# Kernel tuning notes

Measured on AMD Instinct MI355X. Metric: run time of the kernel, lower is better.

## Reference

```python
import jax, jax.numpy as jnp
import numpy as np
import math

B, S, H = 2, 2048, 3072
N_HEADS, N_KV_HEADS, HEAD_DIM = 32, 8, 96
ROPE_THETA = 10000.0
OP_SIZE = N_HEADS * HEAD_DIM + 2 * N_KV_HEADS * HEAD_DIM  # 4608


def setup_inputs() -> dict:
    key = jax.random.key(0)
    k1, k2, k3 = jax.random.split(key, 3)
    hidden_states = jax.random.normal(k1, (B, S, H), dtype=jnp.float32)
    # additive causal mask: 0 on/below diagonal, -inf-ish above
    neg = jnp.finfo(jnp.float32).min
    causal = jnp.where(jnp.tril(jnp.ones((S, S), dtype=bool)), 0.0, neg)
    attention_mask = jnp.broadcast_to(causal[None, None], (B, 1, S, S)).astype(jnp.float32)
    # torch nn.Linear convention: weight [out_features, in_features]
    w_qkv = jax.random.normal(k2, (OP_SIZE, H), dtype=jnp.float32) * 0.02
    w_o = jax.random.normal(k3, (H, H), dtype=jnp.float32) * 0.02
    position_ids = jnp.broadcast_to(jnp.arange(S, dtype=jnp.int32)[None], (B, S))
    return {"hidden_states": hidden_states, "attention_mask": attention_mask,
            "w_qkv": w_qkv, "w_o": w_o, "position_ids": position_ids}


def _rotate_half(x):
    half = x.shape[-1] // 2
    return jnp.concatenate([-x[..., half:], x[..., :half]], axis=-1)


def _rope_cos_sin(position_ids, head_dim, theta):
    # Phi3RotaryEmbedding (no scaling)
    inv_freq = 1.0 / (theta ** (jnp.arange(0, head_dim, 2, dtype=jnp.float32) / head_dim))
    freqs = position_ids.astype(jnp.float32)[:, :, None] * inv_freq[None, None, :]  # [b,s,d/2]
    emb = jnp.concatenate([freqs, freqs], axis=-1)  # [b,s,d]
    return jnp.cos(emb), jnp.sin(emb)


def reference(hidden_states, attention_mask, w_qkv, w_o, position_ids):
    b, s, _ = hidden_states.shape
    qkv = jnp.einsum('bsh,oh->bso', hidden_states, w_qkv)  # quantized qkv_proj (fp emulation)
    q_pos = N_HEADS * HEAD_DIM
    kv_pos = q_pos + N_KV_HEADS * HEAD_DIM
    q = qkv[..., :q_pos].reshape(b, s, N_HEADS, HEAD_DIM).transpose(0, 2, 1, 3)
    k = qkv[..., q_pos:kv_pos].reshape(b, s, N_KV_HEADS, HEAD_DIM).transpose(0, 2, 1, 3)
    v = qkv[..., kv_pos:].reshape(b, s, N_KV_HEADS, HEAD_DIM).transpose(0, 2, 1, 3)

    cos, sin = _rope_cos_sin(position_ids, HEAD_DIM, ROPE_THETA)
    cos, sin = cos[:, None], sin[:, None]  # [b,1,s,d]
    q = q * cos + _rotate_half(q) * sin
    k = k * cos + _rotate_half(k) * sin

    # repeat_kv: GQA expand kv heads to query heads
    groups = N_HEADS // N_KV_HEADS
    k = jnp.repeat(k, groups, axis=1)  # [b,h,s,d]
    v = jnp.repeat(v, groups, axis=1)

    # quantized QK^T matmul (fp emulation)
    scores = jnp.einsum('bhqd,bhkd->bhqk', q, k) / math.sqrt(HEAD_DIM)
    scores = scores + attention_mask  # additive causal mask
    attn = jax.nn.softmax(scores.astype(jnp.float32), axis=-1).astype(v.dtype)
    # dropout p=0 (eval); quantized attn @ V matmul (fp emulation)
    out = jnp.einsum('bhqk,bhkd->bhqd', attn, v)
    out = out.transpose(0, 2, 1, 3).reshape(b, s, N_HEADS * HEAD_DIM)
    out = jnp.einsum('bso,ho->bsh', out, w_o)  # quantized o_proj
    return out
```

## Files before the change

kernel.cpp:

```cpp
#include <hip/hip_runtime.h>
#include <hip/hip_bf16.h>
#include <math.h>

#define S_LEN 2048
#define HDIM  3072
#define NH    32
#define NKV   8
#define HD    96
#define OPSZ  4608
#define QPOS  3072
#define KPOS  3840

typedef short  short8 __attribute__((ext_vector_type(8)));
typedef short  short4v __attribute__((ext_vector_type(4)));
typedef float  f32x4  __attribute__((ext_vector_type(4)));
typedef unsigned short us4 __attribute__((ext_vector_type(4)));

typedef __attribute__((address_space(1))) const unsigned int* gas1_t;
typedef __attribute__((address_space(3))) unsigned int* las3_t;

__device__ __forceinline__ void gl_lds16(const void* g, void* l) {
  __builtin_amdgcn_global_load_lds((gas1_t)g, (las3_t)l, 16, 0, 0);
}

#define VMCNT(n) asm volatile("s_waitcnt vmcnt(" #n ")" ::: "memory")

__device__ __forceinline__ unsigned short f2b(float f) {
  union { float f; unsigned u; } x; x.f = f;
  unsigned r = x.u + 0x7fffu + ((x.u >> 16) & 1u);
  return (unsigned short)(r >> 16);
}
__device__ __forceinline__ float b2f(unsigned short b) {
  union { unsigned u; float f; } x; x.u = ((unsigned)b) << 16;
  return x.f;
}

__device__ __forceinline__ short4v pack_bf16_4(float p0, float p1, float p2, float p3) {
  unsigned u0 = __builtin_bit_cast(unsigned, p0) + 0x8000u;
  unsigned u1 = __builtin_bit_cast(unsigned, p1) + 0x8000u;
  unsigned u2 = __builtin_bit_cast(unsigned, p2) + 0x8000u;
  unsigned u3 = __builtin_bit_cast(unsigned, p3) + 0x8000u;
  unsigned lo = __builtin_amdgcn_perm(u1, u0, 0x07060302u);
  unsigned hi = __builtin_amdgcn_perm(u3, u2, 0x07060302u);
  uint2 q; q.x = lo; q.y = hi;
  return __builtin_bit_cast(short4v, q);
}

__global__ __launch_bounds__(256) void k_convert3(const float* __restrict__ s0, int n0,
                                                  const float* __restrict__ s1, int n1,
                                                  const float* __restrict__ s2, int n2,
                                                  unsigned short* __restrict__ dst) {
  int i = blockIdx.x * 256 + threadIdx.x;
  const float* src; int local;
  if (i < n0)            { src = s0; local = i; }
  else if (i < n0 + n1)  { src = s1; local = i - n0; }
  else if (i < n0 + n1 + n2) { src = s2; local = i - n0 - n1; }
  else return;
  float4 v = ((const float4*)src)[local];
  us4 o;
  o[0] = f2b(v.x); o[1] = f2b(v.y); o[2] = f2b(v.z); o[3] = f2b(v.w);
  ((us4*)dst)[i] = o;
}

template<int OUTBF, int NF>
__global__ __launch_bounds__(512, 2) void k_gemm_pipe(const unsigned short* __restrict__ A,
                                                      const unsigned short* __restrict__ Bt,
                                                      void* __restrict__ Cout,
                                                      int M, int N, int K, int GX) {
  constexpr int BN    = NF * 32;
  constexpr int GSLOT = 8192 + BN * 32;
  __shared__ unsigned short lds[4 * GSLOT];

  const int NC = K >> 5;
  const int tid = threadIdx.x;
  const int lane = tid & 63;
  const int wave = tid >> 6;
  const int wm = wave & 3, wn = wave >> 2;
  const int lr = lane & 15, lg = lane >> 4;
  const int prh = lr >> 1, bit = lr & 1;

  const int nwg = gridDim.x;
  const int id  = blockIdx.x;
  const int sw  = (id & 7) * (nwg >> 3) + (id >> 3);
  const int bx  = sw % GX, by = sw / GX;
  const int m0 = by * 256, n0 = bx * BN;

  const int i0 = tid, i1 = 512 + tid;
  const int p0 = i0 >> 3, g0 = (i0 & 7) ^ (p0 & 7);
  const int p1 = i1 >> 3, g1 = (i1 & 7) ^ (p1 & 7);
  const unsigned short* aG0 = A + (size_t)(m0 + 2 * p0 + (g0 >> 2)) * K + (g0 & 3) * 8;
  const unsigned short* aG1 = A + (size_t)(m0 + 2 * p1 + (g1 >> 2)) * K + (g1 & 3) * 8;
  const int aO0 = i0 * 8, aO1 = i1 * 8;

  const int q0 = i0 >> 3, h0 = (i0 & 7) ^ (q0 & 7);
  const int q1 = i1 >> 3, h1 = (i1 & 7) ^ (q1 & 7);
  const unsigned short* bG0 = Bt + (size_t)(n0 + 2 * q0 + (h0 >> 2)) * K + (h0 & 3) * 8;
  const unsigned short* bG1 = Bt + (size_t)(n0 + 2 * q1 + (h1 >> 2)) * K + (h1 & 3) * 8;
  const int bO0 = 8192 + i0 * 8, bO1 = 8192 + i1 * 8;
  const int i2 = 1024 + (tid & 127);
  const int q2 = i2 >> 3, h2 = (i2 & 7) ^ (q2 & 7);
  const unsigned short* bG2 = Bt + (size_t)(n0 + 2 * q2 + (h2 >> 2)) * K + (h2 & 3) * 8;
  const int bO2 = 8192 + i2 * 8;
  const bool xb = (NF == 9) ? (tid < 128) : (tid < 256);

  auto stageA = [&](int c) {
    unsigned short* sb = &lds[(c & 3) * GSLOT];
    gl_lds16(aG0 + c * 32, sb + aO0);
    gl_lds16(aG1 + c * 32, sb + aO1);
  };
  auto stageB = [&](int c) {
    unsigned short* sb = &lds[(c & 3) * GSLOT];
    gl_lds16(bG0 + c * 32, sb + bO0);
    if constexpr (NF == 9) {
      gl_lds16(bG1 + c * 32, sb + bO1);
      if (xb) gl_lds16(bG2 + c * 32, sb + bO2);
    } else {
      if (xb) gl_lds16(bG1 + c * 32, sb + bO1);
    }
  };

  const int gp  = ((bit << 2) + lg) ^ prh;
  const int aRd = wm * 2048 + prh * 64 + gp * 8;
  const int bRd = 8192 + wn * (BN * 16) + prh * 64 + gp * 8;

  f32x4 acc[4][NF];
#pragma unroll
  for (int mf = 0; mf < 4; mf++)
#pragma unroll
    for (int nf = 0; nf < NF; nf++)
#pragma unroll
      for (int r = 0; r < 4; r++) acc[mf][nf][r] = 0.0f;

#define VM_STEADY() do { \
    if constexpr (NF == 9) { if (wave < 2) { VMCNT(10); } else { VMCNT(8); } } \
    else                   { if (wave < 4) { VMCNT(8);  } else { VMCNT(6); } } } while (0)
#define VM_TAIL1() do { \
    if constexpr (NF == 9) { if (wave < 2) { VMCNT(5); } else { VMCNT(4); } } \
    else                   { if (wave < 4) { VMCNT(4); } else { VMCNT(3); } } } while (0)

  stageA(0); stageB(0);
  stageA(1); stageB(1);
  stageA(2); stageB(2);
  VM_STEADY();
  __builtin_amdgcn_s_barrier();
  __builtin_amdgcn_sched_barrier(0);

  for (int c = 0; c < NC; ++c) {
    const unsigned short* sb = &lds[(c & 3) * GSLOT];
    short8 af[4], bf[NF];
#pragma unroll
    for (int mf = 0; mf < 4; mf++) af[mf] = *(const short8*)&sb[aRd + mf * 512];
#pragma unroll
    for (int nf = 0; nf < NF; nf++) bf[nf] = *(const short8*)&sb[bRd + nf * 512];
    if (c + 3 < NC) { stageA(c + 3); stageB(c + 3); }
    __builtin_amdgcn_s_setprio(1);
#pragma unroll
    for (int nf = 0; nf < NF; nf++)
#pragma unroll
      for (int mf = 0; mf < 4; mf++)
        acc[mf][nf] = __builtin_amdgcn_mfma_f32_16x16x32_bf16(af[mf], bf[nf], acc[mf][nf], 0, 0, 0);
    __builtin_amdgcn_s_setprio(0);
    if (c < NC - 3)       { VM_STEADY(); }
    else if (c == NC - 3) { VM_TAIL1(); }
    else if (c == NC - 2) { VMCNT(0); }
    if (c + 1 < NC) {
      __builtin_amdgcn_sched_barrier(0);
      __builtin_amdgcn_s_barrier();
      __builtin_amdgcn_sched_barrier(0);
    }
  }

#pragma unroll
  for (int mf = 0; mf < 4; mf++)
#pragma unroll
    for (int nf = 0; nf < NF; nf++)
#pragma unroll
      for (int r = 0; r < 4; r++) {
        int row = m0 + wm * 64 + mf * 16 + lg * 4 + r;
        int col = n0 + wn * (BN / 2) + nf * 16 + lr;
        if (OUTBF) ((unsigned short*)Cout)[(size_t)row * N + col] = f2b(acc[mf][nf][r]);
        else       ((float*)Cout)[(size_t)row * N + col] = acc[mf][nf][r];
      }
#undef VM_STEADY
#undef VM_TAIL1
}

__global__ __launch_bounds__(256) void k_rope(const unsigned short* __restrict__ qkv,
                                              const int* __restrict__ pos_ids,
                                              unsigned short* __restrict__ Qb,
                                              unsigned short* __restrict__ Kb) {
  __shared__ float cs[96], sn[96];
  int blk = blockIdx.x;
  int b = blk >> 11, s = blk & 2047;
  int t = threadIdx.x;
  int pos = pos_ids[blk];
  if (t < 48) {
    float e = -((float)(2 * t) / 96.0f) * 9.210340371976184f;
    float invf = __expf(e);
    float a = (float)pos * invf;
    float c, si;
    __sincosf(a, &si, &c);
    cs[t] = c; cs[t + 48] = c;
    sn[t] = si; sn[t + 48] = si;
  }
  __syncthreads();
  const unsigned short* row = qkv + (size_t)blk * OPSZ;
  const float qscale = 0.1020620726159658f;
  for (int o = t; o < KPOS; o += 256) {
    int d = o % 96;
    float x  = b2f(row[o]);
    float xp = b2f(row[d < 48 ? o + 48 : o - 48]);
    float rot = (d < 48) ? -xp : xp;
    float val = x * cs[d] + rot * sn[d];
    if (o < QPOS) {
      int h = o / 96;
      Qb[((size_t)(b * NH + h) * S_LEN + s) * HD + d] = f2b(val * qscale);
    } else {
      int kh = (o - QPOS) / 96;
      Kb[((size_t)(b * NKV + kh) * S_LEN + s) * HD + d] = f2b(val);
    }
  }
}

__global__ __launch_bounds__(256) void k_vtrans(const unsigned short* __restrict__ qkv,
                                                unsigned short* __restrict__ Vt) {
  int blk = blockIdx.x;
  int st = blk & 31, kh = (blk >> 5) & 7, b = blk >> 8;
  int s0 = st * 64;
  __shared__ unsigned short tile[96][65];
  int t = threadIdx.x;
#pragma unroll
  for (int c = 0; c < 24; c++) {
    int idx = c * 256 + t;
    int ls = idx / 96, d = idx % 96;
    tile[d][ls] = qkv[(size_t)(b * S_LEN + s0 + ls) * OPSZ + KPOS + kh * 96 + d];
  }
  __syncthreads();
#pragma unroll
  for (int c = 0; c < 24; c++) {
    int idx = c * 256 + t;
    int d = idx >> 6, ls = idx & 63;
    Vt[((size_t)(b * NKV + kh) * HD + d) * S_LEN + s0 + ls] = tile[d][ls];
  }
}

__global__ __launch_bounds__(512, 4) void k_flash(const unsigned short* __restrict__ Qb,
                                                  const unsigned short* __restrict__ Kb,
                                                  const unsigned short* __restrict__ Vt,
                                                  unsigned short* __restrict__ attn) {
  __shared__ unsigned short smem[36864];
  __shared__ float Lsh[128 * 8];
  unsigned short* QPs = smem + 24576;
  float* Osh = (float*)smem;

  int blk = blockIdx.x;
  int j = blk & 7;
  int h = (blk >> 3) & 31;
  int b = blk >> 8;
  int kh = h >> 2;
  int tid = threadIdx.x, lane = tid & 63, wave = tid >> 6;
  int lr = lane & 15, lg = lane >> 4;
  int qg = wave >> 1, kg = wave & 1;
  const int swz = (lr >> 1) & 3;

  const unsigned short* ksrc = Kb + (size_t)(b * NKV + kh) * S_LEN * HD;
  const unsigned short* vsrc = Vt + (size_t)(b * NKV + kh) * HD * S_LEN;

  auto stageKV = [&](int it, int sl) {
    int k0 = it * 64;
    unsigned short* Ksl = smem + sl * 6144;
    unsigned short* Vsl = smem + 12288 + sl * 6144;
#pragma unroll
    for (int p = 0; p < 3; p++) {
      int gi = p * 512 + tid;
      if (gi < 768) {
        int pl = gi >> 8, wp = gi & 255;
        int r = wp >> 2, s = wp & 3;
        int l = pl * 4 + (s ^ ((r >> 1) & 3));
        gl_lds16(ksrc + (size_t)(k0 + r) * HD + l * 8, &Ksl[gi * 8]);
      } else {
        int gi2 = gi - 768;
        int pl = (gi2 >= 384) ? 1 : 0;
        int rem = gi2 - pl * 384;
        int d = rem >> 2, s = rem & 3;
        int l = s ^ ((d >> 1) & 3);
        gl_lds16(vsrc + (size_t)d * S_LEN + k0 + pl * 32 + l * 8, &Vsl[gi2 * 8]);
      }
    }
  };

  for (int half = 0; half < 2; half++) {
    int qtile = half ? (15 - j) : j;
    int q0 = qtile * 128;
    const unsigned short* qsrc = Qb + ((size_t)(b * NH + h) * S_LEN + q0) * HD;
    int nk = qtile * 2 + 2;

    __syncthreads();
#pragma unroll
    for (int p = 0; p < 3; p++) {
      int gi = p * 512 + tid;
      int pl = gi >> 9, wp = gi & 511;
      int r = wp >> 2, s = wp & 3;
      int l = pl * 4 + (s ^ ((r >> 1) & 3));
      gl_lds16(qsrc + (size_t)r * HD + l * 8, &QPs[gi * 8]);
    }
    stageKV(0, 0);
    stageKV(1, 1);
    VMCNT(3);
    __builtin_amdgcn_s_barrier();
    __builtin_amdgcn_sched_barrier(0);

    short8 qf[2][3];
#pragma unroll
    for (int qt = 0; qt < 2; qt++)
#pragma unroll
      for (int ds = 0; ds < 3; ds++)
        qf[qt][ds] = *(const short8*)&QPs[ds * 4096 + (qg * 32 + qt * 16 + lr) * 32 + (lg ^ swz) * 8];

    f32x4 oacc[2][6];
#pragma unroll
    for (int qt = 0; qt < 2; qt++)
#pragma unroll
      for (int dt = 0; dt < 6; dt++)
#pragma unroll
        for (int r = 0; r < 4; r++) oacc[qt][dt][r] = 0.0f;
    float lsum[2] = {0.0f, 0.0f};

    for (int it = 0; it < nk; it++) {
      int sl = it & 1;
      const unsigned short* Ksl = smem + sl * 6144;
      const unsigned short* Vsl = smem + 12288 + sl * 6144;
      if (it >= 1 && it + 1 < nk) stageKV(it + 1, (it + 1) & 1);
      int k0 = it * 64;
      f32x4 sc[2][2];
#pragma unroll
      for (int kt = 0; kt < 2; kt++)
#pragma unroll
        for (int qt = 0; qt < 2; qt++)
#pragma unroll
          for (int r = 0; r < 4; r++) sc[kt][qt][r] = 0.0f;
#pragma unroll
      for (int kt = 0; kt < 2; kt++)
#pragma unroll
        for (int ds = 0; ds < 3; ds++) {
          short8 kf = *(const short8*)&Ksl[ds * 2048 + (kg * 32 + kt * 16 + lr) * 32 + (lg ^ swz) * 8];
#pragma unroll
          for (int qt = 0; qt < 2; qt++)
            sc[kt][qt] = __builtin_amdgcn_mfma_f32_16x16x32_bf16(kf, qf[qt][ds], sc[kt][qt], 0, 0, 0);
        }
      if (it >= nk - 2) {
#pragma unroll
        for (int kt = 0; kt < 2; kt++)
#pragma unroll
          for (int qt = 0; qt < 2; qt++) {
            int qrow = q0 + qg * 32 + qt * 16 + lr;
            int keyb = k0 + kg * 32 + kt * 16 + lg * 4;
#pragma unroll
            for (int r = 0; r < 4; r++)
              if (keyb + r > qrow) sc[kt][qt][r] = -3.0e38f;
          }
      }
      short4v pf[2][2];
#pragma unroll
      for (int kt = 0; kt < 2; kt++)
#pragma unroll
        for (int qt = 0; qt < 2; qt++) {
          float p0 = __expf(sc[kt][qt][0]);
          float p1 = __expf(sc[kt][qt][1]);
          float p2 = __expf(sc[kt][qt][2]);
          float p3 = __expf(sc[kt][qt][3]);
          lsum[qt] += (p0 + p1) + (p2 + p3);
          pf[kt][qt] = pack_bf16_4(p0, p1, p2, p3);
        }
#pragma unroll
      for (int kt = 0; kt < 2; kt++)
#pragma unroll
        for (int dt = 0; dt < 6; dt++) {
          short4v vf = *(const short4v*)&Vsl[kg * 3072 + (dt * 16 + lr) * 32 +
                                            (((kt * 2 + (lg >> 1)) ^ swz) * 8) + (lg & 1) * 4];
#pragma unroll
          for (int qt = 0; qt < 2; qt++)
            oacc[qt][dt] = __builtin_amdgcn_mfma_f32_16x16x16bf16_1k(pf[kt][qt], vf, oacc[qt][dt], 0, 0, 0);
        }
      VMCNT(0);
      __builtin_amdgcn_sched_barrier(0);
      __builtin_amdgcn_s_barrier();
      __builtin_amdgcn_sched_barrier(0);
    }
    if (kg == 0) {
#pragma unroll
      for (int qt = 0; qt < 2; qt++)
#pragma unroll
        for (int dt = 0; dt < 6; dt++)
#pragma unroll
          for (int r = 0; r < 4; r++)
            Osh[(qg * 32 + qt * 16 + lg * 4 + r) * 97 + dt * 16 + lr] = oacc[qt][dt][r];
    }
#pragma unroll
    for (int qt = 0; qt < 2; qt++)
      Lsh[(qg * 32 + qt * 16 + lr) * 8 + kg * 4 + lg] = lsum[qt];
    __syncthreads();
    if (kg == 1) {
      float linv[2][4];
#pragma unroll
      for (int qt = 0; qt < 2; qt++)
#pragma unroll
        for (int r = 0; r < 4; r++) {
          int row = qg * 32 + qt * 16 + lg * 4 + r;
          float4 a = *(const float4*)&Lsh[row * 8];
          float4 c = *(const float4*)&Lsh[row * 8 + 4];
          linv[qt][r] = 1.0f / ((a.x + a.y + a.z + a.w) + (c.x + c.y + c.z + c.w));
        }
#pragma unroll
      for (int qt = 0; qt < 2; qt++)
#pragma unroll
        for (int dt = 0; dt < 6; dt++)
#pragma unroll
          for (int r = 0; r < 4; r++) {
            int rowl = qg * 32 + qt * 16 + lg * 4 + r;
            float v = Osh[rowl * 97 + dt * 16 + lr] + oacc[qt][dt][r];
            int row = q0 + rowl;
            int col = h * 96 + dt * 16 + lr;
            attn[(size_t)(b * S_LEN + row) * HDIM + col] = f2b(v * linv[qt][r]);
          }
    }
  }
}

extern "C" void kernel_launch(void* const* d_in, const int* in_sizes, int n_in,
                              void* d_out, int out_size, void* d_ws, size_t ws_size,
                              hipStream_t stream) {
  const float* hidden = (const float*)d_in[0];
  const float* w_qkv  = (const float*)d_in[2];
  const float* w_o    = (const float*)d_in[3];
  const int*   posids = (const int*)d_in[4];

  const size_t M = 4096;
  unsigned short* hidden_bf = (unsigned short*)d_ws;
  unsigned short* wqkv_bf   = hidden_bf + M * HDIM;
  unsigned short* wo_bf     = wqkv_bf + (size_t)OPSZ * HDIM;
  unsigned short* qkv_bf    = wo_bf + (size_t)HDIM * HDIM;
  unsigned short* Qb   = hidden_bf;
  unsigned short* Kb   = wqkv_bf;
  unsigned short* Vt   = wqkv_bf + (size_t)NKV * 2 * S_LEN * HD;
  unsigned short* attn = qkv_bf;

  int n4h = (int)(M * HDIM / 4);
  int n4q = (int)((size_t)OPSZ * HDIM / 4);
  int n4o = (int)((size_t)HDIM * HDIM / 4);
  int n4t = n4h + n4q + n4o;
  k_convert3<<<(n4t + 255) / 256, 256, 0, stream>>>(hidden, n4h, w_qkv, n4q, w_o, n4o,
                                                    hidden_bf);

  k_gemm_pipe<1, 9><<<256, 512, 0, stream>>>(hidden_bf, wqkv_bf, qkv_bf,
                                             (int)M, OPSZ, HDIM, OPSZ / 288);
  k_rope<<<(int)M, 256, 0, stream>>>(qkv_bf, posids, Qb, Kb);
  k_vtrans<<<2 * NKV * (S_LEN / 64), 256, 0, stream>>>(qkv_bf, Vt);
  k_flash<<<2 * NH * 8, 512, 0, stream>>>(Qb, Kb, Vt, attn);
  k_gemm_pipe<0, 6><<<256, 512, 0, stream>>>(attn, wo_bf, d_out,
                                             (int)M, HDIM, HDIM, HDIM / 192);
}
```

Measured before the change: 482.3 us.

## Stagger GEMM MFMA clusters per wave and unroll flash loop by two

In the GEMM, waves in the two N halves now issue their MFMA work in opposite halves first, with matching B-fragment load order and sched barriers. The aim is to desynchronise the waves so LDS reads overlap MFMA execution. In the flash kernel, the KV loop is unrolled by two with fixed LDS buffer pointers, and the staging address arithmetic is precomputed into incrementing pointers and offset tables. This removes per-iteration index math and slot selection, at the cost of more registers and larger code.

New measurement: 509.2 us. 5.6% more time.

```diff
diff --git a/kernel.cpp b/kernel.cpp
--- a/kernel.cpp
+++ b/kernel.cpp
@@ -69,6 +69,7 @@
                                                       int M, int N, int K, int GX) {
   constexpr int BN    = NF * 32;
   constexpr int GSLOT = 8192 + BN * 32;
+  constexpr int NFA   = (NF + 1) / 2;
   __shared__ unsigned short lds[4 * GSLOT];
 
   const int NC = K >> 5;
@@ -138,6 +139,19 @@
     if constexpr (NF == 9) { if (wave < 2) { VMCNT(5); } else { VMCNT(4); } } \
     else                   { if (wave < 4) { VMCNT(4); } else { VMCNT(3); } } } while (0)
 
+#define CLUSTER_A() do { \
+    __builtin_amdgcn_s_setprio(1); \
+    _Pragma("unroll") for (int nf = 0; nf < NFA; nf++) \
+      _Pragma("unroll") for (int mf = 0; mf < 4; mf++) \
+        acc[mf][nf] = __builtin_amdgcn_mfma_f32_16x16x32_bf16(af[mf], bf[nf], acc[mf][nf], 0, 0, 0); \
+    __builtin_amdgcn_s_setprio(0); } while (0)
+#define CLUSTER_B() do { \
+    __builtin_amdgcn_s_setprio(1); \
+    _Pragma("unroll") for (int nf = NFA; nf < NF; nf++) \
+      _Pragma("unroll") for (int mf = 0; mf < 4; mf++) \
+        acc[mf][nf] = __builtin_amdgcn_mfma_f32_16x16x32_bf16(af[mf], bf[nf], acc[mf][nf], 0, 0, 0); \
+    __builtin_amdgcn_s_setprio(0); } while (0)
+
   stageA(0); stageB(0);
   stageA(1); stageB(1);
   stageA(2); stageB(2);
@@ -150,16 +164,26 @@
     short8 af[4], bf[NF];
 #pragma unroll
     for (int mf = 0; mf < 4; mf++) af[mf] = *(const short8*)&sb[aRd + mf * 512];
-#pragma unroll
-    for (int nf = 0; nf < NF; nf++) bf[nf] = *(const short8*)&sb[bRd + nf * 512];
+    if (wn == 0) {
+#pragma unroll
+      for (int nf = 0; nf < NF; nf++) bf[nf] = *(const short8*)&sb[bRd + nf * 512];
+    } else {
+#pragma unroll
+      for (int nf = NFA; nf < NF; nf++) bf[nf] = *(const short8*)&sb[bRd + nf * 512];
+#pragma unroll
+      for (int nf = 0; nf < NFA; nf++) bf[nf] = *(const short8*)&sb[bRd + nf * 512];
+    }
     if (c + 3 < NC) { stageA(c + 3); stageB(c + 3); }
-    __builtin_amdgcn_s_setprio(1);
-#pragma unroll
-    for (int nf = 0; nf < NF; nf++)
-#pragma unroll
-      for (int mf = 0; mf < 4; mf++)
-        acc[mf][nf] = __builtin_amdgcn_mfma_f32_16x16x32_bf16(af[mf], bf[nf], acc[mf][nf], 0, 0, 0);
-    __builtin_amdgcn_s_setprio(0);
+    __builtin_amdgcn_sched_barrier(0);
+    if (wn == 0) {
+      CLUSTER_A();
+      __builtin_amdgcn_sched_barrier(0);
+      CLUSTER_B();
+    } else {
+      CLUSTER_B();
+      __builtin_amdgcn_sched_barrier(0);
+      CLUSTER_A();
+    }
     if (c < NC - 3)       { VM_STEADY(); }
     else if (c == NC - 3) { VM_TAIL1(); }
     else if (c == NC - 2) { VMCNT(0); }
@@ -183,6 +207,8 @@
       }
 #undef VM_STEADY
 #undef VM_TAIL1
+#undef CLUSTER_A
+#undef CLUSTER_B
 }
 
 __global__ __launch_bounds__(256) void k_rope(const unsigned short* __restrict__ qkv,
@@ -250,7 +276,11 @@
                                                   unsigned short* __restrict__ attn) {
   __shared__ unsigned short smem[36864];
   __shared__ float Lsh[128 * 8];
-  unsigned short* QPs = smem + 24576;
+  unsigned short* const K0 = smem;
+  unsigned short* const K1 = smem + 6144;
+  unsigned short* const V0 = smem + 12288;
+  unsigned short* const V1 = smem + 18432;
+  unsigned short* const QPs = smem + 24576;
   float* Osh = (float*)smem;
 
   int blk = blockIdx.x;
@@ -266,34 +296,100 @@
   const unsigned short* ksrc = Kb + (size_t)(b * NKV + kh) * S_LEN * HD;
   const unsigned short* vsrc = Vt + (size_t)(b * NKV + kh) * HD * S_LEN;
 
-  auto stageKV = [&](int it, int sl) {
-    int k0 = it * 64;
-    unsigned short* Ksl = smem + sl * 6144;
-    unsigned short* Vsl = smem + 12288 + sl * 6144;
-#pragma unroll
-    for (int p = 0; p < 3; p++) {
-      int gi = p * 512 + tid;
-      if (gi < 768) {
-        int pl = gi >> 8, wp = gi & 255;
-        int r = wp >> 2, s = wp & 3;
-        int l = pl * 4 + (s ^ ((r >> 1) & 3));
-        gl_lds16(ksrc + (size_t)(k0 + r) * HD + l * 8, &Ksl[gi * 8]);
-      } else {
-        int gi2 = gi - 768;
-        int pl = (gi2 >= 384) ? 1 : 0;
-        int rem = gi2 - pl * 384;
-        int d = rem >> 2, s = rem & 3;
-        int l = s ^ ((d >> 1) & 3);
-        gl_lds16(vsrc + (size_t)d * S_LEN + k0 + pl * 32 + l * 8, &Vsl[gi2 * 8]);
-      }
-    }
-  };
+  const int gA = tid, plA = gA >> 8, wpA = gA & 255, rA = wpA >> 2, sA = wpA & 3;
+  const int lA = plA * 4 + (sA ^ ((rA >> 1) & 3));
+  const unsigned short* const kb0 = ksrc + (size_t)rA * HD + lA * 8;
+  const int rB = (tid & 255) >> 2, sB = tid & 3;
+  const int lB = 8 + (sB ^ ((rB >> 1) & 3));
+  const unsigned short* const kb1 = ksrc + (size_t)rB * HD + lB * 8;
+  const int gC = tid & 255, dC = gC >> 2, sC = gC & 3;
+  const int lC = sC ^ ((dC >> 1) & 3);
+  const unsigned short* const vb1 = vsrc + (size_t)dC * S_LEN + lC * 8;
+  const int gD = 256 + tid, plD = (gD >= 384) ? 1 : 0, remD = gD - plD * 384;
+  const int dD = remD >> 2, sD = remD & 3;
+  const int lD = sD ^ ((dD >> 1) & 3);
+  const unsigned short* const vb2 = vsrc + (size_t)dD * S_LEN + plD * 32 + lD * 8;
+  const int o0 = tid * 8, o1k = (512 + tid) * 8, o1v = (tid - 256) * 8, o2 = (256 + tid) * 8;
+
+  const unsigned short* kp0;
+  const unsigned short* kp1;
+  const unsigned short* vp1;
+  const unsigned short* vp2;
+
+#define FSTAGE(KD, VD) do {                                                   \
+    gl_lds16(kp0, (KD) + o0);                                                 \
+    if (tid < 256) gl_lds16(kp1, (KD) + o1k);                                 \
+    else           gl_lds16(vp1, (VD) + o1v);                                 \
+    gl_lds16(vp2, (VD) + o2);                                                 \
+    kp0 += 64 * HD; kp1 += 64 * HD; vp1 += 64; vp2 += 64;                     \
+  } while (0)
+
+  int koff[2][3], voff[2][6];
+#pragma unroll
+  for (int kt = 0; kt < 2; kt++) {
+#pragma unroll
+    for (int ds = 0; ds < 3; ds++)
+      koff[kt][ds] = ds * 2048 + (kg * 32 + kt * 16 + lr) * 32 + (lg ^ swz) * 8;
+#pragma unroll
+    for (int dt = 0; dt < 6; dt++)
+      voff[kt][dt] = kg * 3072 + (dt * 16 + lr) * 32 +
+                     (((kt * 2 + (lg >> 1)) ^ swz) * 8) + (lg & 1) * 4;
+  }
+
+#define FCOMP(KSL, VSL, IT, MASKED) do {                                      \
+    f32x4 sc[2][2];                                                           \
+    _Pragma("unroll") for (int kt = 0; kt < 2; kt++)                          \
+      _Pragma("unroll") for (int qt = 0; qt < 2; qt++)                        \
+        _Pragma("unroll") for (int r = 0; r < 4; r++) sc[kt][qt][r] = 0.0f;   \
+    _Pragma("unroll") for (int kt = 0; kt < 2; kt++)                          \
+      _Pragma("unroll") for (int ds = 0; ds < 3; ds++) {                      \
+        short8 kf = *(const short8*)&(KSL)[koff[kt][ds]];                     \
+        _Pragma("unroll") for (int qt = 0; qt < 2; qt++)                      \
+          sc[kt][qt] = __builtin_amdgcn_mfma_f32_16x16x32_bf16(kf, qf[qt][ds], sc[kt][qt], 0, 0, 0); \
+      }                                                                       \
+    if (MASKED) {                                                             \
+      int k0m = (IT) * 64;                                                    \
+      _Pragma("unroll") for (int kt = 0; kt < 2; kt++)                        \
+        _Pragma("unroll") for (int qt = 0; qt < 2; qt++) {                    \
+          int qrow = q0 + qg * 32 + qt * 16 + lr;                             \
+          int keyb = k0m + kg * 32 + kt * 16 + lg * 4;                        \
+          _Pragma("unroll") for (int r = 0; r < 4; r++)                       \
+            if (keyb + r > qrow) sc[kt][qt][r] = -3.0e38f;                    \
+        }                                                                     \
+    }                                                                         \
+    short4v pf[2][2];                                                         \
+    _Pragma("unroll") for (int kt = 0; kt < 2; kt++)                          \
+      _Pragma("unroll") for (int qt = 0; qt < 2; qt++) {                      \
+        float pp0 = __expf(sc[kt][qt][0]);                                    \
+        float pp1 = __expf(sc[kt][qt][1]);                                    \
+        float pp2 = __expf(sc[kt][qt][2]);                                    \
+        float pp3 = __expf(sc[kt][qt][3]);                                    \
+        lsum[qt] += (pp0 + pp1) + (pp2 + pp3);                                \
+        pf[kt][qt] = pack_bf16_4(pp0, pp1, pp2, pp3);                         \
+      }                                                                       \
+    _Pragma("unroll") for (int kt = 0; kt < 2; kt++)                          \
+      _Pragma("unroll") for (int dt = 0; dt < 6; dt++) {                      \
+        short4v vf = *(const short4v*)&(VSL)[voff[kt][dt]];                   \
+        _Pragma("unroll") for (int qt = 0; qt < 2; qt++)                      \
+          oacc[qt][dt] = __builtin_amdgcn_mfma_f32_16x16x16bf16_1k(pf[kt][qt], vf, oacc[qt][dt], 0, 0, 0); \
+      }                                                                       \
+  } while (0)
+
+#define FSYNC() do {                                                          \
+    VMCNT(0);                                                                 \
+    __builtin_amdgcn_sched_barrier(0);                                        \
+    __builtin_amdgcn_s_barrier();                                             \
+    __builtin_amdgcn_sched_barrier(0);                                        \
+  } while (0)
 
   for (int half = 0; half < 2; half++) {
     int qtile = half ? (15 - j) : j;
     int q0 = qtile * 128;
     const unsigned short* qsrc = Qb + ((size_t)(b * NH + h) * S_LEN + q0) * HD;
     int nk = qtile * 2 + 2;
+    int nb = nk >> 1;
+
+    kp0 = kb0; kp1 = kb1; vp1 = vb1; vp2 = vb2;
 
     __syncthreads();
 #pragma unroll
@@ -304,8 +400,8 @@
       int l = pl * 4 + (s ^ ((r >> 1) & 3));
       gl_lds16(qsrc + (size_t)r * HD + l * 8, &QPs[gi * 8]);
     }
-    stageKV(0, 0);
-    stageKV(1, 1);
+    FSTAGE(K0, V0);
+    FSTAGE(K1, V1);
     VMCNT(3);
     __builtin_amdgcn_s_barrier();
     __builtin_amdgcn_sched_barrier(0);
@@ -326,67 +422,16 @@
         for (int r = 0; r < 4; r++) oacc[qt][dt][r] = 0.0f;
     float lsum[2] = {0.0f, 0.0f};
 
-    for (int it = 0; it < nk; it++) {
-      int sl = it & 1;
-      const unsigned short* Ksl = smem + sl * 6144;
-      const unsigned short* Vsl = smem + 12288 + sl * 6144;
-      if (it >= 1 && it + 1 < nk) stageKV(it + 1, (it + 1) & 1);
-      int k0 = it * 64;
-      f32x4 sc[2][2];
-#pragma unroll
-      for (int kt = 0; kt < 2; kt++)
-#pragma unroll
-        for (int qt = 0; qt < 2; qt++)
-#pragma unroll
-          for (int r = 0; r < 4; r++) sc[kt][qt][r] = 0.0f;
-#pragma unroll
-      for (int kt = 0; kt < 2; kt++)
-#pragma unroll
-        for (int ds = 0; ds < 3; ds++) {
-          short8 kf = *(const short8*)&Ksl[ds * 2048 + (kg * 32 + kt * 16 + lr) * 32 + (lg ^ swz) * 8];
-#pragma unroll
-          for (int qt = 0; qt < 2; qt++)
-            sc[kt][qt] = __builtin_amdgcn_mfma_f32_16x16x32_bf16(kf, qf[qt][ds], sc[kt][qt], 0, 0, 0);
-        }
-      if (it >= nk - 2) {
-#pragma unroll
-        for (int kt = 0; kt < 2; kt++)
-#pragma unroll
-          for (int qt = 0; qt < 2; qt++) {
-            int qrow = q0 + qg * 32 + qt * 16 + lr;
-            int keyb = k0 + kg * 32 + kt * 16 + lg * 4;
-#pragma unroll
-            for (int r = 0; r < 4; r++)
-              if (keyb + r > qrow) sc[kt][qt][r] = -3.0e38f;
-          }
-      }
-      short4v pf[2][2];
-#pragma unroll
-      for (int kt = 0; kt < 2; kt++)
-#pragma unroll
-        for (int qt = 0; qt < 2; qt++) {
-          float p0 = __expf(sc[kt][qt][0]);
-          float p1 = __expf(sc[kt][qt][1]);
-          float p2 = __expf(sc[kt][qt][2]);
-          float p3 = __expf(sc[kt][qt][3]);
-          lsum[qt] += (p0 + p1) + (p2 + p3);
-          pf[kt][qt] = pack_bf16_4(p0, p1, p2, p3);
-        }
-#pragma unroll
-      for (int kt = 0; kt < 2; kt++)
-#pragma unroll
-        for (int dt = 0; dt < 6; dt++) {
-          short4v vf = *(const short4v*)&Vsl[kg * 3072 + (dt * 16 + lr) * 32 +
-                                            (((kt * 2 + (lg >> 1)) ^ swz) * 8) + (lg & 1) * 4];
-#pragma unroll
-          for (int qt = 0; qt < 2; qt++)
-            oacc[qt][dt] = __builtin_amdgcn_mfma_f32_16x16x16bf16_1k(pf[kt][qt], vf, oacc[qt][dt], 0, 0, 0);
-        }
-      VMCNT(0);
-      __builtin_amdgcn_sched_barrier(0);
-      __builtin_amdgcn_s_barrier();
-      __builtin_amdgcn_sched_barrier(0);
-    }
+    for (int bi = 0; bi < nb; bi++) {
+      const bool mk = (bi == nb - 1);
+      if (bi > 0) FSTAGE(K1, V1);
+      FCOMP(K0, V0, 2 * bi, mk);
+      FSYNC();
+      if (2 * bi + 2 < nk) FSTAGE(K0, V0);
+      FCOMP(K1, V1, 2 * bi + 1, mk);
+      FSYNC();
+    }
+
     if (kg == 0) {
 #pragma unroll
       for (int qt = 0; qt < 2; qt++)
@@ -425,6 +470,9 @@
           }
     }
   }
+#undef FSTAGE
+#undef FCOMP
+#undef FSYNC
 }
 
 extern "C" void kernel_launch(void* const* d_in, const int* in_sizes, int n_in,
```
